# Performance work log

Measured on AMD Instinct MI355X. Metric: run time of the kernel, lower is better.

Reference implementation:

```python
import jax, jax.numpy as jnp
import numpy as np


def _conv(x, w, b, stride=1, pad=0):
    y = jax.lax.conv_general_dilated(
        x, w, (stride, stride), [(pad, pad), (pad, pad)],
        dimension_numbers=('NCHW', 'OIHW', 'NCHW'))
    return y + b[None, :, None, None]


def _channel_mask(x, w, b):
    # SE-style hard channel mask: GAP -> linear -> hard threshold at 0
    pooled = jnp.mean(x, axis=(2, 3))                 # [B, Cin]
    logits = pooled @ w.T + b                         # [B, Cout]
    return (logits > 0).astype(x.dtype)[:, :, None, None]


def _maxpool3(m):
    # 3x3 stride-1 dilation of the binary spatial mask
    return jax.lax.reduce_window(m, -jnp.inf, jax.lax.max,
                                 (1, 1, 3, 3), (1, 1, 1, 1),
                                 [(0, 0), (0, 0), (1, 1), (1, 1)])


def _hswish(x):
    return x * jax.nn.relu6(x + 3.0) / 6.0


def _coord_att(x, w1, b1, wh, bh, ww, bw):
    B, C, H, W = x.shape
    xh = jnp.mean(x, axis=3, keepdims=True)                         # [B,C,H,1]
    xw = jnp.mean(x, axis=2, keepdims=True).transpose(0, 1, 3, 2)   # [B,C,W,1]
    y = _hswish(_conv(jnp.concatenate([xh, xw], axis=2), w1, b1))   # [B,mip,H+W,1]
    yh, yw = y[:, :, :H], y[:, :, H:]
    ah = jax.nn.sigmoid(_conv(yh, wh, bh))                          # [B,C,H,1]
    aw = jax.nn.sigmoid(_conv(yw, ww, bw)).transpose(0, 1, 3, 2)    # [B,C,1,W]
    return x * ah * aw


def setup_inputs() -> dict:
    key = jax.random.key(0)
    ks = jax.random.split(key, 16)
    B, INP, WID, OUP, H, W, MIP = 16, 512, 128, 512, 56, 56, 16
    f32 = jnp.float32
    rn = lambda k, s, sc: jax.random.normal(k, s, f32) * sc
    return {
        'x': rn(ks[0], (B, INP, H, W), 1.0),
        # spatial mask unit (1x1 conv to 1-channel logits)
        'sm_w': rn(ks[1], (1, INP, 1, 1), 0.05), 'sm_b': jnp.zeros((1,), f32),
        # channel mask units (GAP + linear)
        'cm1_w': rn(ks[2], (WID, INP), 0.05), 'cm1_b': jnp.zeros((WID,), f32),
        'cm2_w': rn(ks[3], (WID, WID), 0.09), 'cm2_b': jnp.zeros((WID,), f32),
        'cm3_w': rn(ks[4], (OUP, WID), 0.09), 'cm3_b': jnp.zeros((OUP,), f32),
        # bottleneck convs
        'w1': rn(ks[5], (WID, INP, 1, 1), 0.044), 'b1': jnp.zeros((WID,), f32),
        'w2': rn(ks[6], (WID, WID, 3, 3), 0.029), 'b2': jnp.zeros((WID,), f32),
        'w3': rn(ks[7], (OUP, WID, 1, 1), 0.088), 'b3': jnp.zeros((OUP,), f32),
        # coordinate attention
        'ca_w1': rn(ks[8], (MIP, OUP, 1, 1), 0.044), 'ca_b1': jnp.zeros((MIP,), f32),
        'ca_wh': rn(ks[9], (OUP, MIP, 1, 1), 0.25), 'ca_bh': jnp.zeros((OUP,), f32),
        'ca_ww': rn(ks[10], (OUP, MIP, 1, 1), 0.25), 'ca_bw': jnp.zeros((OUP,), f32),
    }


def reference(x, sm_w, sm_b, cm1_w, cm1_b, cm2_w, cm2_b, cm3_w, cm3_b,
              w1, b1, w2, b2, w3, b3,
              ca_w1, ca_b1, ca_wh, ca_bh, ca_ww, ca_bw):
    identity = x
    # spatial masks: std + 3x3-dilated
    s_mask = (_conv(x, sm_w, sm_b) > 0).astype(x.dtype)   # [B,1,H,W]
    s_mask_dil = _maxpool3(s_mask)
    # conv1: 1x1 + ReLU, gated by channel mask 1 and dilated spatial mask
    cm1 = _channel_mask(x, cm1_w, cm1_b)
    h = jax.nn.relu(_conv(x, w1, b1)) * cm1 * s_mask_dil
    # conv2: 3x3 + ReLU, gated by channel mask 2 and std spatial mask
    cm2 = _channel_mask(h, cm2_w, cm2_b)
    h = jax.nn.relu(_conv(h, w2, b2, pad=1)) * cm2 * s_mask
    # conv3: 1x1, no activation, gated by channel mask 3 and std spatial mask
    cm3 = _channel_mask(h, cm3_w, cm3_b)
    h = _conv(h, w3, b3) * cm3 * s_mask
    # coordinate attention + residual
    out = _coord_att(h, ca_w1, ca_b1, ca_wh, ca_bh, ca_ww, ca_bw)
    return jax.nn.relu(out + identity)
```

## Files before the change

kernel.cpp:

```cpp
#include <hip/hip_runtime.h>

#define HWn 3136
#define W56 56
#define Bn  16
#define CIN0 512

typedef unsigned short ushortT;
typedef __attribute__((ext_vector_type(8))) short bf16x8;
typedef __attribute__((ext_vector_type(4))) float f32x4;

__device__ inline ushortT bf_hi(float v) {
    unsigned u = __float_as_uint(v);
    unsigned r = u + 0x7FFFu + ((u >> 16) & 1u);
    return (ushortT)(r >> 16);
}
__device__ inline float bf_f(ushortT h) { return __uint_as_float(((unsigned)h) << 16); }

__global__ __launch_bounds__(256) void pool_mean_kernel(const float* __restrict__ in,
                                                        float* __restrict__ out)
{
    int bc = blockIdx.x;
    const float* p = in + (size_t)bc * HWn;
    float s = 0.f;
    for (int i = threadIdx.x; i < HWn; i += 256) s += p[i];
#pragma unroll
    for (int off = 32; off > 0; off >>= 1) s += __shfl_down(s, off);
    __shared__ float red[4];
    if ((threadIdx.x & 63) == 0) red[threadIdx.x >> 6] = s;
    __syncthreads();
    if (threadIdx.x == 0) out[bc] = (red[0] + red[1] + red[2] + red[3]) / 3136.f;
}

__global__ void zero_kernel(float* __restrict__ p, int n)
{
    int i = blockIdx.x * 256 + threadIdx.x;
    if (i < n) p[i] = 0.f;
}

__global__ __launch_bounds__(256) void pool_meanT_kernel(const ushortT* __restrict__ hi,
        const ushortT* __restrict__ lo, float* __restrict__ pooled)
{
    int b = blockIdx.x, slice = blockIdx.y;
    int t = threadIdx.x;
    int c4 = (t & 31) * 4, rg = t >> 5;
    float a0 = 0.f, a1 = 0.f, a2 = 0.f, a3 = 0.f;
    for (int it = 0; it < 49; ++it) {
        int p = slice * 392 + rg + it * 8;
        size_t base = ((size_t)b * HWn + p) * 128 + c4;
        ushort4 h4 = *(const ushort4*)&hi[base];
        ushort4 l4 = *(const ushort4*)&lo[base];
        a0 += bf_f(h4.x) + bf_f(l4.x);
        a1 += bf_f(h4.y) + bf_f(l4.y);
        a2 += bf_f(h4.z) + bf_f(l4.z);
        a3 += bf_f(h4.w) + bf_f(l4.w);
    }
    __shared__ float red[8][128];
    red[rg][c4] = a0; red[rg][c4 + 1] = a1; red[rg][c4 + 2] = a2; red[rg][c4 + 3] = a3;
    __syncthreads();
    if (t < 128) {
        float s = 0.f;
#pragma unroll
        for (int g = 0; g < 8; ++g) s += red[g][t];
        atomicAdd(&pooled[b * 128 + t], s * (1.f / 3136.f));
    }
}

__global__ void chan_mask_kernel(const float* __restrict__ pooled, const float* __restrict__ Wm,
                                 const float* __restrict__ bias, float* __restrict__ mask,
                                 int Cin, int Cout)
{
    int b = blockIdx.x, o = threadIdx.x;
    if (o >= Cout) return;
    const float* pr = pooled + (size_t)b * Cin;
    const float* wr = Wm + (size_t)o * Cin;
    float s = bias[o];
    for (int c = 0; c < Cin; ++c) s = fmaf(pr[c], wr[c], s);
    mask[b * Cout + o] = (s > 0.f) ? 1.f : 0.f;
}

__global__ __launch_bounds__(256) void spatial_mask_kernel(const float* __restrict__ x,
        const float* __restrict__ smw, const float* __restrict__ smb, float* __restrict__ smask)
{
    __shared__ float ws[512];
    int b = blockIdx.x;
    for (int i = threadIdx.x; i < 512; i += 256) ws[i] = smw[i];
    __syncthreads();
    int p = blockIdx.y * 256 + threadIdx.x;
    if (p >= HWn) return;
    const float* xp = x + (size_t)b * CIN0 * HWn + p;
    float s = smb[0];
#pragma unroll 8
    for (int c = 0; c < CIN0; ++c) s = fmaf(xp[(size_t)c * HWn], ws[c], s);
    smask[b * HWn + p] = (s > 0.f) ? 1.f : 0.f;
}

__global__ __launch_bounds__(256) void dilate_kernel(const float* __restrict__ sm, float* __restrict__ sd)
{
    int b = blockIdx.x;
    int p = blockIdx.y * 256 + threadIdx.x;
    if (p >= HWn) return;
    int py = p / W56, px = p % W56;
    float m = 0.f;
    for (int dy = -1; dy <= 1; ++dy) {
        int sy = py + dy; if (sy < 0 || sy >= W56) continue;
        for (int dx = -1; dx <= 1; ++dx) {
            int sx = px + dx; if (sx < 0 || sx >= W56) continue;
            m = fmaxf(m, sm[b * HWn + sy * W56 + sx]);
        }
    }
    sd[b * HWn + p] = m;
}

__global__ void split_w_kernel(const float* __restrict__ w, ushortT* __restrict__ hi,
                               ushortT* __restrict__ lo, int n)
{
    int i = blockIdx.x * 256 + threadIdx.x;
    if (i >= n) return;
    float v = w[i];
    ushortT h = bf_hi(v);
    hi[i] = h;
    lo[i] = bf_hi(v - bf_f(h));
}

__global__ void split_w2_kernel(const float* __restrict__ w2, ushortT* __restrict__ hi,
                                ushortT* __restrict__ lo)
{
    int e = blockIdx.x * 256 + threadIdx.x;
    if (e >= 9 * 128 * 128) return;
    int c = e & 127, o = (e >> 7) & 127, tap = e >> 14;
    float v = w2[((size_t)o * 128 + c) * 9 + tap];
    ushortT h = bf_hi(v);
    hi[e] = h;
    lo[e] = bf_hi(v - bf_f(h));
}

template<int KC, int TAPS, bool RELU, bool IN_F32, bool OUT_F32>
__global__ __launch_bounds__(256) void mfma_conv_kernel(
    const float* __restrict__ in_f32,
    const ushortT* __restrict__ in_hi, const ushortT* __restrict__ in_lo,
    const ushortT* __restrict__ wh, const ushortT* __restrict__ wl,
    const float* __restrict__ bias, const float* __restrict__ cmask,
    const float* __restrict__ pmask,
    float* __restrict__ out_f32, ushortT* __restrict__ out_hi, ushortT* __restrict__ out_lo,
    int Cout)
{
    __shared__ __align__(16) ushortT As_hi[128 * 40], As_lo[128 * 40];
    __shared__ __align__(16) ushortT Bs_hi[128 * 40], Bs_lo[128 * 40];
    __shared__ float s_bias[128], s_cm[128];

    const int b  = blockIdx.z;
    const int o0 = blockIdx.y * 128;
    const int p0 = blockIdx.x * 128;
    const int tid = threadIdx.x;
    const int lane = tid & 63;
    const int g  = lane >> 4;
    const int lc = lane & 15;
    const int wid = tid >> 6;
    const int wm = wid >> 1, wn = wid & 1;

    if (tid < 128) {
        s_bias[tid] = bias[o0 + tid];
        s_cm[tid]   = cmask[b * Cout + o0 + tid];
    }

    int aoff[4], boff[4];
#pragma unroll
    for (int m = 0; m < 4; ++m) aoff[m] = (wm * 64 + m * 16 + lc) * 40 + g * 8;
#pragma unroll
    for (int n = 0; n < 4; ++n) {
        int pl = wn * 64 + n * 16 + lc;
        boff[n] = pl * 40 + ((g ^ (pl & 3)) * 8);
    }

    f32x4 acc[4][4];
#pragma unroll
    for (int m = 0; m < 4; ++m)
#pragma unroll
        for (int n = 0; n < 4; ++n) acc[m][n] = (f32x4){0.f, 0.f, 0.f, 0.f};

    for (int tap = 0; tap < TAPS; ++tap) {
        const int dy = (TAPS == 9) ? (tap / 3 - 1) : 0;
        const int dx = (TAPS == 9) ? (tap % 3 - 1) : 0;
        for (int kc = 0; kc < KC; kc += 32) {
            __syncthreads();
#pragma unroll
            for (int i = 0; i < 2; ++i) {
                int unit = tid + i * 256;
                int row = unit >> 2, ch = unit & 3;
                size_t srow = (TAPS == 9) ? ((size_t)tap * 128 + row) * 128
                                          : (size_t)(o0 + row) * KC;
                uint4 vh = *(const uint4*)(wh + srow + kc + ch * 8);
                uint4 vl = *(const uint4*)(wl + srow + kc + ch * 8);
                *(uint4*)&As_hi[row * 40 + ch * 8] = vh;
                *(uint4*)&As_lo[row * 40 + ch * 8] = vl;
            }
            if (IN_F32) {
                const float* inB = in_f32 + (size_t)b * KC * HWn;
#pragma unroll
                for (int j = 0; j < 4; ++j) {
                    int cr = (tid >> 5) + j * 8;
                    int p4 = (tid & 31) * 4;
                    float4 xv = make_float4(0.f, 0.f, 0.f, 0.f);
                    if (p0 + p4 < HWn)
                        xv = *(const float4*)&inB[(size_t)(kc + cr) * HWn + p0 + p4];
                    float vv[4] = {xv.x, xv.y, xv.z, xv.w};
#pragma unroll
                    for (int e = 0; e < 4; ++e) {
                        int prow = p4 + e;
                        ushortT h = bf_hi(vv[e]);
                        ushortT l = bf_hi(vv[e] - bf_f(h));
                        int kk = ((cr >> 3) ^ (prow & 3)) * 8 + (cr & 7);
                        Bs_hi[prow * 40 + kk] = h;
                        Bs_lo[prow * 40 + kk] = l;
                    }
                }
            } else {
#pragma unroll
                for (int i = 0; i < 2; ++i) {
                    int unit = tid + i * 256;
                    int row = unit >> 2, ch = unit & 3;
                    int pg = p0 + row;
                    int q = pg, valid;
                    if (TAPS == 9) {
                        int py = pg / 56, px = pg % 56;
                        int sy = py + dy, sx = px + dx;
                        valid = (pg < HWn) && (sy >= 0) && (sy < 56) && (sx >= 0) && (sx < 56);
                        q = sy * 56 + sx;
                    } else {
                        valid = (pg < HWn);
                    }
                    uint4 vh = make_uint4(0u, 0u, 0u, 0u), vl = vh;
                    if (valid) {
                        size_t sbase = ((size_t)b * HWn + q) * 128 + kc + ch * 8;
                        vh = *(const uint4*)(in_hi + sbase);
                        vl = *(const uint4*)(in_lo + sbase);
                    }
                    int chs = ch ^ (row & 3);
                    *(uint4*)&Bs_hi[row * 40 + chs * 8] = vh;
                    *(uint4*)&Bs_lo[row * 40 + chs * 8] = vl;
                }
            }
            __syncthreads();
            bf16x8 a_h[4], a_l[4];
#pragma unroll
            for (int m = 0; m < 4; ++m) {
                a_h[m] = *(const bf16x8*)&As_hi[aoff[m]];
                a_l[m] = *(const bf16x8*)&As_lo[aoff[m]];
            }
#pragma unroll
            for (int n = 0; n < 4; ++n) {
                bf16x8 b_h = *(const bf16x8*)&Bs_hi[boff[n]];
                bf16x8 b_l = *(const bf16x8*)&Bs_lo[boff[n]];
#pragma unroll
                for (int m = 0; m < 4; ++m) {
                    acc[m][n] = __builtin_amdgcn_mfma_f32_16x16x32_bf16(a_h[m], b_h, acc[m][n], 0, 0, 0);
                    acc[m][n] = __builtin_amdgcn_mfma_f32_16x16x32_bf16(a_h[m], b_l, acc[m][n], 0, 0, 0);
                    acc[m][n] = __builtin_amdgcn_mfma_f32_16x16x32_bf16(a_l[m], b_h, acc[m][n], 0, 0, 0);
                }
            }
        }
    }

#pragma unroll
    for (int m = 0; m < 4; ++m) {
        int ob = wm * 64 + m * 16 + g * 4;
        f32x4 b4 = *(const f32x4*)&s_bias[ob];
        f32x4 c4 = *(const f32x4*)&s_cm[ob];
#pragma unroll
        for (int n = 0; n < 4; ++n) {
            int p = p0 + wn * 64 + n * 16 + lc;
            if (p >= HWn) continue;
            float pm = pmask[b * HWn + p];
            float v[4];
#pragma unroll
            for (int r = 0; r < 4; ++r) {
                float t = acc[m][n][r] + b4[r];
                if (RELU) t = fmaxf(t, 0.f);
                v[r] = t * c4[r] * pm;
            }
            if (OUT_F32) {
#pragma unroll
                for (int r = 0; r < 4; ++r)
                    out_f32[((size_t)b * Cout + o0 + ob + r) * HWn + p] = v[r];
            } else {
                ushort4 H, L;
                H.x = bf_hi(v[0]); L.x = bf_hi(v[0] - bf_f(H.x));
                H.y = bf_hi(v[1]); L.y = bf_hi(v[1] - bf_f(H.y));
                H.z = bf_hi(v[2]); L.z = bf_hi(v[2] - bf_f(H.z));
                H.w = bf_hi(v[3]); L.w = bf_hi(v[3] - bf_f(H.w));
                size_t base = ((size_t)b * HWn + p) * 128 + ob;
                *(ushort4*)&out_hi[base] = H;
                *(ushort4*)&out_lo[base] = L;
            }
        }
    }
}

__global__ __launch_bounds__(128) void rowcol_mean_kernel(const float* __restrict__ h3,
        float* __restrict__ xh, float* __restrict__ xw)
{
    __shared__ float t[HWn];
    int bc = blockIdx.x;
    const float* p = h3 + (size_t)bc * HWn;
    for (int i = threadIdx.x; i < HWn; i += 128) t[i] = p[i];
    __syncthreads();
    int tid = threadIdx.x;
    if (tid < 56) {
        float s = 0.f;
#pragma unroll
        for (int i = 0; i < 56; ++i) s += t[tid * 56 + i];
        xh[(size_t)bc * 56 + tid] = s / 56.f;
    } else if (tid >= 64 && tid < 120) {
        int c = tid - 64;
        float s = 0.f;
#pragma unroll
        for (int i = 0; i < 56; ++i) s += t[i * 56 + c];
        xw[(size_t)bc * 56 + c] = s / 56.f;
    }
}

__global__ __launch_bounds__(256) void ca_y_kernel(const float* __restrict__ xh,
        const float* __restrict__ xw, const float* __restrict__ w1c,
        const float* __restrict__ b1c, float* __restrict__ y)
{
    int b = blockIdx.x;
    int t = blockIdx.y;
    __shared__ float src[512];
    __shared__ float part[16][17];
    for (int c = threadIdx.x; c < 512; c += 256)
        src[c] = (t < 56) ? xh[((size_t)b * 512 + c) * 56 + t]
                          : xw[((size_t)b * 512 + c) * 56 + (t - 56)];
    __syncthreads();
    int m  = threadIdx.x & 15;
    int cp = threadIdx.x >> 4;
    float s = 0.f;
#pragma unroll 8
    for (int i = 0; i < 32; ++i) {
        int c = cp * 32 + i;
        s = fmaf(w1c[(size_t)m * 512 + c], src[c], s);
    }
    part[m][cp] = s;
    __syncthreads();
    if (threadIdx.x < 16) {
        float v = b1c[threadIdx.x];
#pragma unroll
        for (int i = 0; i < 16; ++i) v += part[threadIdx.x][i];
        float r6 = fminf(fmaxf(v + 3.f, 0.f), 6.f);
        y[((size_t)b * 16 + threadIdx.x) * 112 + t] = v * r6 / 6.f;
    }
}

__global__ __launch_bounds__(512) void ca_a_kernel(const float* __restrict__ y,
        const float* __restrict__ wh, const float* __restrict__ bh,
        const float* __restrict__ wwp, const float* __restrict__ bw,
        float* __restrict__ ah, float* __restrict__ aw)
{
    int r = blockIdx.x;
    int side = blockIdx.y;
    int b = blockIdx.z;
    int o = threadIdx.x;
    __shared__ float ys[16];
    if (threadIdx.x < 16)
        ys[threadIdx.x] = y[((size_t)b * 16 + threadIdx.x) * 112 + side * 56 + r];
    __syncthreads();
    const float* wmat = side ? wwp : wh;
    float s = (side ? bw : bh)[o];
#pragma unroll
    for (int m = 0; m < 16; ++m) s = fmaf(wmat[o * 16 + m], ys[m], s);
    float sig = 1.f / (1.f + expf(-s));
    (side ? aw : ah)[((size_t)b * 512 + o) * 56 + r] = sig;
}

__global__ __launch_bounds__(256) void finalize_kernel(const float* __restrict__ x,
        const float* __restrict__ ah, const float* __restrict__ aw, float* __restrict__ out)
{
    int e = blockIdx.x * 256 + threadIdx.x;
    int pq = e % 784;
    int bc = e / 784;
    int p = pq * 4;
    int py = p / 56, px = p % 56;
    float4 h = *((const float4*)out + e);
    float4 xv = *((const float4*)x + e);
    float a_h = ah[(size_t)bc * 56 + py];
    float4 a_w = *(const float4*)&aw[(size_t)bc * 56 + px];
    float4 v;
    v.x = fmaxf(h.x * a_h * a_w.x + xv.x, 0.f);
    v.y = fmaxf(h.y * a_h * a_w.y + xv.y, 0.f);
    v.z = fmaxf(h.z * a_h * a_w.z + xv.z, 0.f);
    v.w = fmaxf(h.w * a_h * a_w.w + xv.w, 0.f);
    *((float4*)out + e) = v;
}

extern "C" void kernel_launch(void* const* d_in, const int* in_sizes, int n_in,
                              void* d_out, int out_size, void* d_ws, size_t ws_size,
                              hipStream_t stream)
{
    (void)in_sizes; (void)n_in; (void)out_size; (void)ws_size;
    const float* x     = (const float*)d_in[0];
    const float* sm_w  = (const float*)d_in[1];
    const float* sm_b  = (const float*)d_in[2];
    const float* cm1_w = (const float*)d_in[3];
    const float* cm1_b = (const float*)d_in[4];
    const float* cm2_w = (const float*)d_in[5];
    const float* cm2_b = (const float*)d_in[6];
    const float* cm3_w = (const float*)d_in[7];
    const float* cm3_b = (const float*)d_in[8];
    const float* w1    = (const float*)d_in[9];
    const float* b1    = (const float*)d_in[10];
    const float* w2    = (const float*)d_in[11];
    const float* b2    = (const float*)d_in[12];
    const float* w3    = (const float*)d_in[13];
    const float* b3    = (const float*)d_in[14];
    const float* ca_w1 = (const float*)d_in[15];
    const float* ca_b1 = (const float*)d_in[16];
    const float* ca_wh = (const float*)d_in[17];
    const float* ca_bh = (const float*)d_in[18];
    const float* ca_ww = (const float*)d_in[19];
    const float* ca_bw = (const float*)d_in[20];
    float* out = (float*)d_out;

    float* fp = (float*)d_ws;
    float* pooled_x  = fp;              fp += 8192;
    float* cm1m      = fp;              fp += 2048;
    float* smask     = fp;              fp += 50176;
    float* sdil      = fp;              fp += 50176;
    float* pooled_h1 = fp;              fp += 2048;
    float* cm2m      = fp;              fp += 2048;
    float* pooled_h2 = fp;              fp += 2048;
    float* cm3m      = fp;              fp += 8192;
    ushortT* up = (ushortT*)fp;
    ushortT* w1h = up;                  up += 65536;
    ushortT* w1l = up;                  up += 65536;
    ushortT* w2h = up;                  up += 147456;
    ushortT* w2l = up;                  up += 147456;
    ushortT* w3h = up;                  up += 65536;
    ushortT* w3l = up;                  up += 65536;
    ushortT* h1h = up;                  up += 6422528;
    ushortT* h1l = up;                  up += 6422528;
    ushortT* h2h = up;                  up += 6422528;
    ushortT* h2l = up;                  up += 6422528;
    float* xh  = (float*)h1h;
    float* xwm = xh + 458752;
    float* yb  = xwm + 458752;
    float* ah  = yb + 28672;
    float* aw  = ah + 458752;

    zero_kernel<<<8, 256, 0, stream>>>(pooled_h1, 2048);
    zero_kernel<<<8, 256, 0, stream>>>(pooled_h2, 2048);
    pool_mean_kernel<<<Bn * CIN0, 256, 0, stream>>>(x, pooled_x);
    chan_mask_kernel<<<Bn, 128, 0, stream>>>(pooled_x, cm1_w, cm1_b, cm1m, 512, 128);
    spatial_mask_kernel<<<dim3(Bn, 13), 256, 0, stream>>>(x, sm_w, sm_b, smask);
    dilate_kernel<<<dim3(Bn, 13), 256, 0, stream>>>(smask, sdil);
    split_w_kernel<<<256, 256, 0, stream>>>(w1, w1h, w1l, 65536);
    split_w2_kernel<<<576, 256, 0, stream>>>(w2, w2h, w2l);
    split_w_kernel<<<256, 256, 0, stream>>>(w3, w3h, w3l, 65536);

    mfma_conv_kernel<512, 1, true, true, false><<<dim3(25, 1, Bn), 256, 0, stream>>>(
        x, nullptr, nullptr, w1h, w1l, b1, cm1m, sdil, nullptr, h1h, h1l, 128);

    pool_meanT_kernel<<<dim3(Bn, 8), 256, 0, stream>>>(h1h, h1l, pooled_h1);
    chan_mask_kernel<<<Bn, 128, 0, stream>>>(pooled_h1, cm2_w, cm2_b, cm2m, 128, 128);

    mfma_conv_kernel<128, 9, true, false, false><<<dim3(25, 1, Bn), 256, 0, stream>>>(
        nullptr, h1h, h1l, w2h, w2l, b2, cm2m, smask, nullptr, h2h, h2l, 128);

    pool_meanT_kernel<<<dim3(Bn, 8), 256, 0, stream>>>(h2h, h2l, pooled_h2);
    chan_mask_kernel<<<Bn, 512, 0, stream>>>(pooled_h2, cm3_w, cm3_b, cm3m, 128, 512);

    mfma_conv_kernel<128, 1, false, false, true><<<dim3(25, 4, Bn), 256, 0, stream>>>(
        nullptr, h2h, h2l, w3h, w3l, b3, cm3m, smask, out, nullptr, nullptr, 512);

    rowcol_mean_kernel<<<Bn * 512, 128, 0, stream>>>(out, xh, xwm);
    ca_y_kernel<<<dim3(Bn, 112), 256, 0, stream>>>(xh, xwm, ca_w1, ca_b1, yb);
    ca_a_kernel<<<dim3(W56, 2, Bn), 512, 0, stream>>>(yb, ca_wh, ca_bh, ca_ww, ca_bw, ah, aw);
    finalize_kernel<<<25088, 256, 0, stream>>>(x, ah, aw, out);
}
```

Measured before the change: 663.5 us.

## Fuse spatial-mask logits with channel pooling and shrink conv tiles to 64 outputs

Replaces the separate global-average-pool and spatial-mask kernels with one tiled kernel that reads x once, computes partial spatial logits per 64-channel slice and per-channel sums via atomics, followed by a small threshold kernel. The MFMA conv kernel moves from 256-thread 128x128 tiles to 128-thread 64x128 tiles, doubling the grid. It also removes the LDS XOR swizzle and rewrites the fp32 input staging so each thread packs channel pairs. This should cut redundant passes over x and raise block count, but dropping the swizzle may bring back LDS bank conflicts and the partial-logit buffer adds extra traffic.

```diff
diff --git a/kernel.cpp b/kernel.cpp
--- a/kernel.cpp
+++ b/kernel.cpp
@@ -16,25 +16,83 @@
 }
 __device__ inline float bf_f(ushortT h) { return __uint_as_float(((unsigned)h) << 16); }
 
-__global__ __launch_bounds__(256) void pool_mean_kernel(const float* __restrict__ in,
-                                                        float* __restrict__ out)
-{
-    int bc = blockIdx.x;
-    const float* p = in + (size_t)bc * HWn;
-    float s = 0.f;
-    for (int i = threadIdx.x; i < HWn; i += 256) s += p[i];
-#pragma unroll
-    for (int off = 32; off > 0; off >>= 1) s += __shfl_down(s, off);
-    __shared__ float red[4];
-    if ((threadIdx.x & 63) == 0) red[threadIdx.x >> 6] = s;
-    __syncthreads();
-    if (threadIdx.x == 0) out[bc] = (red[0] + red[1] + red[2] + red[3]) / 3136.f;
-}
-
 __global__ void zero_kernel(float* __restrict__ p, int n)
 {
     int i = blockIdx.x * 256 + threadIdx.x;
     if (i < n) p[i] = 0.f;
+}
+
+__global__ __launch_bounds__(256) void mask_pool_kernel(
+    const float* __restrict__ x, const float* __restrict__ smw,
+    float* __restrict__ slog_part, float* __restrict__ pooled)
+{
+    __shared__ float s_t[64][129];
+    __shared__ float s_w[64];
+    __shared__ float s_slog[128];
+    __shared__ float s_pool[4][64];
+    const int b = blockIdx.z, ct = blockIdx.y, pt = blockIdx.x;
+    const int c0 = ct * 64, p0 = pt * 128;
+    const int t = threadIdx.x;
+    if (t < 64) s_w[t] = smw[c0 + t];
+    __syncthreads();
+    const int pi = t & 127, par = t >> 7;
+    const int p = p0 + pi;
+    const bool pv = (p < HWn);
+    const float* xb = x + ((size_t)b * 512 + c0) * HWn;
+    float sacc = 0.f;
+#pragma unroll 4
+    for (int rep = 0; rep < 32; ++rep) {
+        int ci = rep * 2 + par;
+        float v = pv ? xb[(size_t)ci * HWn + p] : 0.f;
+        s_t[ci][pi] = v;
+        sacc = fmaf(v, s_w[ci], sacc);
+    }
+    if (par == 0) s_slog[pi] = sacc;
+    __syncthreads();
+    if (par == 1) s_slog[pi] += sacc;
+    __syncthreads();
+    if (t < 128 && p0 + t < HWn)
+        slog_part[((size_t)b * 8 + ct) * HWn + p0 + t] = s_slog[t];
+    const int c = t & 63, pg = t >> 6;
+    float a = 0.f;
+#pragma unroll 8
+    for (int it = 0; it < 32; ++it) a += s_t[c][pg * 32 + it];
+    s_pool[pg], __syncthreads();
+    s_pool[pg][c] = a;
+    __syncthreads();
+    if (t < 64) {
+        float s = s_pool[0][t] + s_pool[1][t] + s_pool[2][t] + s_pool[3][t];
+        atomicAdd(&pooled[b * 512 + c0 + t], s * (1.f / 3136.f));
+    }
+}
+
+__global__ void thresh_kernel(const float* __restrict__ slog_part,
+                              const float* __restrict__ smb, float* __restrict__ smask)
+{
+    int e = blockIdx.x * 256 + threadIdx.x;
+    if (e >= Bn * HWn) return;
+    int b = e / HWn, p = e % HWn;
+    float s = smb[0];
+#pragma unroll
+    for (int i = 0; i < 8; ++i) s += slog_part[((size_t)b * 8 + i) * HWn + p];
+    smask[e] = (s > 0.f) ? 1.f : 0.f;
+}
+
+__global__ __launch_bounds__(256) void dilate_kernel(const float* __restrict__ sm, float* __restrict__ sd)
+{
+    int b = blockIdx.x;
+    int p = blockIdx.y * 256 + threadIdx.x;
+    if (p >= HWn) return;
+    int py = p / W56, px = p % W56;
+    float m = 0.f;
+    for (int dy = -1; dy <= 1; ++dy) {
+        int sy = py + dy; if (sy < 0 || sy >= W56) continue;
+        for (int dx = -1; dx <= 1; ++dx) {
+            int sx = px + dx; if (sx < 0 || sx >= W56) continue;
+            m = fmaxf(m, sm[b * HWn + sy * W56 + sx]);
+        }
+    }
+    sd[b * HWn + p] = m;
 }
 
 __global__ __launch_bounds__(256) void pool_meanT_kernel(const ushortT* __restrict__ hi,
@@ -78,39 +136,6 @@
     mask[b * Cout + o] = (s > 0.f) ? 1.f : 0.f;
 }
 
-__global__ __launch_bounds__(256) void spatial_mask_kernel(const float* __restrict__ x,
-        const float* __restrict__ smw, const float* __restrict__ smb, float* __restrict__ smask)
-{
-    __shared__ float ws[512];
-    int b = blockIdx.x;
-    for (int i = threadIdx.x; i < 512; i += 256) ws[i] = smw[i];
-    __syncthreads();
-    int p = blockIdx.y * 256 + threadIdx.x;
-    if (p >= HWn) return;
-    const float* xp = x + (size_t)b * CIN0 * HWn + p;
-    float s = smb[0];
-#pragma unroll 8
-    for (int c = 0; c < CIN0; ++c) s = fmaf(xp[(size_t)c * HWn], ws[c], s);
-    smask[b * HWn + p] = (s > 0.f) ? 1.f : 0.f;
-}
-
-__global__ __launch_bounds__(256) void dilate_kernel(const float* __restrict__ sm, float* __restrict__ sd)
-{
-    int b = blockIdx.x;
-    int p = blockIdx.y * 256 + threadIdx.x;
-    if (p >= HWn) return;
-    int py = p / W56, px = p % W56;
-    float m = 0.f;
-    for (int dy = -1; dy <= 1; ++dy) {
-        int sy = py + dy; if (sy < 0 || sy >= W56) continue;
-        for (int dx = -1; dx <= 1; ++dx) {
-            int sx = px + dx; if (sx < 0 || sx >= W56) continue;
-            m = fmaxf(m, sm[b * HWn + sy * W56 + sx]);
-        }
-    }
-    sd[b * HWn + p] = m;
-}
-
 __global__ void split_w_kernel(const float* __restrict__ w, ushortT* __restrict__ hi,
                                ushortT* __restrict__ lo, int n)
 {
@@ -135,7 +160,7 @@
 }
 
 template<int KC, int TAPS, bool RELU, bool IN_F32, bool OUT_F32>
-__global__ __launch_bounds__(256) void mfma_conv_kernel(
+__global__ __launch_bounds__(128) void mfma_conv_kernel(
     const float* __restrict__ in_f32,
     const ushortT* __restrict__ in_hi, const ushortT* __restrict__ in_lo,
     const ushortT* __restrict__ wh, const ushortT* __restrict__ wl,
@@ -144,33 +169,29 @@
     float* __restrict__ out_f32, ushortT* __restrict__ out_hi, ushortT* __restrict__ out_lo,
     int Cout)
 {
-    __shared__ __align__(16) ushortT As_hi[128 * 40], As_lo[128 * 40];
+    __shared__ __align__(16) ushortT As_hi[64 * 40], As_lo[64 * 40];
     __shared__ __align__(16) ushortT Bs_hi[128 * 40], Bs_lo[128 * 40];
-    __shared__ float s_bias[128], s_cm[128];
+    __shared__ float s_bias[64], s_cm[64];
 
     const int b  = blockIdx.z;
-    const int o0 = blockIdx.y * 128;
+    const int o0 = blockIdx.y * 64;
     const int p0 = blockIdx.x * 128;
     const int tid = threadIdx.x;
     const int lane = tid & 63;
     const int g  = lane >> 4;
     const int lc = lane & 15;
-    const int wid = tid >> 6;
-    const int wm = wid >> 1, wn = wid & 1;
-
-    if (tid < 128) {
+    const int wn = tid >> 6;
+
+    if (tid < 64) {
         s_bias[tid] = bias[o0 + tid];
         s_cm[tid]   = cmask[b * Cout + o0 + tid];
     }
 
     int aoff[4], boff[4];
 #pragma unroll
-    for (int m = 0; m < 4; ++m) aoff[m] = (wm * 64 + m * 16 + lc) * 40 + g * 8;
-#pragma unroll
-    for (int n = 0; n < 4; ++n) {
-        int pl = wn * 64 + n * 16 + lc;
-        boff[n] = pl * 40 + ((g ^ (pl & 3)) * 8);
-    }
+    for (int m = 0; m < 4; ++m) aoff[m] = (m * 16 + lc) * 40 + g * 8;
+#pragma unroll
+    for (int n = 0; n < 4; ++n) boff[n] = (wn * 64 + n * 16 + lc) * 40 + g * 8;
 
     f32x4 acc[4][4];
 #pragma unroll
@@ -185,42 +206,37 @@
             __syncthreads();
 #pragma unroll
             for (int i = 0; i < 2; ++i) {
-                int unit = tid + i * 256;
-                int row = unit >> 2, ch = unit & 3;
-                size_t srow = (TAPS == 9) ? ((size_t)tap * 128 + row) * 128
-                                          : (size_t)(o0 + row) * KC;
-                uint4 vh = *(const uint4*)(wh + srow + kc + ch * 8);
-                uint4 vl = *(const uint4*)(wl + srow + kc + ch * 8);
-                *(uint4*)&As_hi[row * 40 + ch * 8] = vh;
-                *(uint4*)&As_lo[row * 40 + ch * 8] = vl;
+                int u = tid + i * 128;
+                int row = u >> 2, ch = u & 3;
+                size_t srow = (TAPS == 9) ? (((size_t)tap * 128 + o0 + row) * 128 + kc)
+                                          : ((size_t)(o0 + row) * KC + kc);
+                *(uint4*)&As_hi[row * 40 + ch * 8] = *(const uint4*)(wh + srow + ch * 8);
+                *(uint4*)&As_lo[row * 40 + ch * 8] = *(const uint4*)(wl + srow + ch * 8);
             }
             if (IN_F32) {
                 const float* inB = in_f32 + (size_t)b * KC * HWn;
-#pragma unroll
-                for (int j = 0; j < 4; ++j) {
-                    int cr = (tid >> 5) + j * 8;
-                    int p4 = (tid & 31) * 4;
-                    float4 xv = make_float4(0.f, 0.f, 0.f, 0.f);
-                    if (p0 + p4 < HWn)
-                        xv = *(const float4*)&inB[(size_t)(kc + cr) * HWn + p0 + p4];
-                    float vv[4] = {xv.x, xv.y, xv.z, xv.w};
-#pragma unroll
-                    for (int e = 0; e < 4; ++e) {
-                        int prow = p4 + e;
-                        ushortT h = bf_hi(vv[e]);
-                        ushortT l = bf_hi(vv[e] - bf_f(h));
-                        int kk = ((cr >> 3) ^ (prow & 3)) * 8 + (cr & 7);
-                        Bs_hi[prow * 40 + kk] = h;
-                        Bs_lo[prow * 40 + kk] = l;
-                    }
+                const int p = tid;
+                const int gp = p0 + p;
+                const bool pv = (gp < HWn);
+                uint* bh32 = (uint*)Bs_hi;
+                uint* bl32 = (uint*)Bs_lo;
+#pragma unroll
+                for (int j = 0; j < 16; ++j) {
+                    float v0 = pv ? inB[(size_t)(kc + 2 * j) * HWn + gp] : 0.f;
+                    float v1 = pv ? inB[(size_t)(kc + 2 * j + 1) * HWn + gp] : 0.f;
+                    ushortT h0 = bf_hi(v0), h1 = bf_hi(v1);
+                    ushortT l0 = bf_hi(v0 - bf_f(h0)), l1 = bf_hi(v1 - bf_f(h1));
+                    bh32[p * 20 + j] = (uint)h0 | ((uint)h1 << 16);
+                    bl32[p * 20 + j] = (uint)l0 | ((uint)l1 << 16);
                 }
             } else {
 #pragma unroll
-                for (int i = 0; i < 2; ++i) {
-                    int unit = tid + i * 256;
-                    int row = unit >> 2, ch = unit & 3;
+                for (int i = 0; i < 4; ++i) {
+                    int u = tid + i * 128;
+                    int row = u >> 2, ch = u & 3;
                     int pg = p0 + row;
-                    int q = pg, valid;
+                    int q = pg;
+                    bool valid;
                     if (TAPS == 9) {
                         int py = pg / 56, px = pg % 56;
                         int sy = py + dy, sx = px + dx;
@@ -231,13 +247,12 @@
                     }
                     uint4 vh = make_uint4(0u, 0u, 0u, 0u), vl = vh;
                     if (valid) {
-                        size_t sbase = ((size_t)b * HWn + q) * 128 + kc + ch * 8;
-                        vh = *(const uint4*)(in_hi + sbase);
-                        vl = *(const uint4*)(in_lo + sbase);
+                        size_t sb = ((size_t)b * HWn + q) * KC + kc + ch * 8;
+                        vh = *(const uint4*)(in_hi + sb);
+                        vl = *(const uint4*)(in_lo + sb);
                     }
-                    int chs = ch ^ (row & 3);
-                    *(uint4*)&Bs_hi[row * 40 + chs * 8] = vh;
-                    *(uint4*)&Bs_lo[row * 40 + chs * 8] = vl;
+                    *(uint4*)&Bs_hi[row * 40 + ch * 8] = vh;
+                    *(uint4*)&Bs_lo[row * 40 + ch * 8] = vl;
                 }
             }
             __syncthreads();
@@ -263,7 +278,7 @@
 
 #pragma unroll
     for (int m = 0; m < 4; ++m) {
-        int ob = wm * 64 + m * 16 + g * 4;
+        int ob = m * 16 + g * 4;
         f32x4 b4 = *(const f32x4*)&s_bias[ob];
         f32x4 c4 = *(const f32x4*)&s_cm[ob];
 #pragma unroll
@@ -288,7 +303,7 @@
                 H.y = bf_hi(v[1]); L.y = bf_hi(v[1] - bf_f(H.y));
                 H.z = bf_hi(v[2]); L.z = bf_hi(v[2] - bf_f(H.z));
                 H.w = bf_hi(v[3]); L.w = bf_hi(v[3] - bf_f(H.w));
-                size_t base = ((size_t)b * HWn + p) * 128 + ob;
+                size_t base = ((size_t)b * HWn + p) * 128 + o0 + ob;
                 *(ushort4*)&out_hi[base] = H;
                 *(ushort4*)&out_lo[base] = L;
             }
@@ -421,13 +436,14 @@
 
     float* fp = (float*)d_ws;
     float* pooled_x  = fp;              fp += 8192;
+    float* pooled_h1 = fp;              fp += 2048;
+    float* pooled_h2 = fp;              fp += 2048;
     float* cm1m      = fp;              fp += 2048;
+    float* cm2m      = fp;              fp += 2048;
+    float* cm3m      = fp;              fp += 8192;
     float* smask     = fp;              fp += 50176;
     float* sdil      = fp;              fp += 50176;
-    float* pooled_h1 = fp;              fp += 2048;
-    float* cm2m      = fp;              fp += 2048;
-    float* pooled_h2 = fp;              fp += 2048;
-    float* cm3m      = fp;              fp += 8192;
+    float* slog_part = fp;              fp += 401408;
     ushortT* up = (ushortT*)fp;
     ushortT* w1h = up;                  up += 65536;
     ushortT* w1l = up;                  up += 65536;
@@ -445,29 +461,28 @@
     float* ah  = yb + 28672;
     float* aw  = ah + 458752;
 
-    zero_kernel<<<8, 256, 0, stream>>>(pooled_h1, 2048);
-    zero_kernel<<<8, 256, 0, stream>>>(pooled_h2, 2048);
-    pool_mean_kernel<<<Bn * CIN0, 256, 0, stream>>>(x, pooled_x);
+    zero_kernel<<<48, 256, 0, stream>>>(pooled_x, 12288);
+    mask_pool_kernel<<<dim3(25, 8, Bn), 256, 0, stream>>>(x, sm_w, slog_part, pooled_x);
+    thresh_kernel<<<196, 256, 0, stream>>>(slog_part, sm_b, smask);
+    dilate_kernel<<<dim3(Bn, 13), 256, 0, stream>>>(smask, sdil);
     chan_mask_kernel<<<Bn, 128, 0, stream>>>(pooled_x, cm1_w, cm1_b, cm1m, 512, 128);
-    spatial_mask_kernel<<<dim3(Bn, 13), 256, 0, stream>>>(x, sm_w, sm_b, smask);
-    dilate_kernel<<<dim3(Bn, 13), 256, 0, stream>>>(smask, sdil);
     split_w_kernel<<<256, 256, 0, stream>>>(w1, w1h, w1l, 65536);
     split_w2_kernel<<<576, 256, 0, stream>>>(w2, w2h, w2l);
     split_w_kernel<<<256, 256, 0, stream>>>(w3, w3h, w3l, 65536);
 
-    mfma_conv_kernel<512, 1, true, true, false><<<dim3(25, 1, Bn), 256, 0, stream>>>(
+    mfma_conv_kernel<512, 1, true, true, false><<<dim3(25, 2, Bn), 128, 0, stream>>>(
         x, nullptr, nullptr, w1h, w1l, b1, cm1m, sdil, nullptr, h1h, h1l, 128);
 
     pool_meanT_kernel<<<dim3(Bn, 8), 256, 0, stream>>>(h1h, h1l, pooled_h1);
     chan_mask_kernel<<<Bn, 128, 0, stream>>>(pooled_h1, cm2_w, cm2_b, cm2m, 128, 128);
 
-    mfma_conv_kernel<128, 9, true, false, false><<<dim3(25, 1, Bn), 256, 0, stream>>>(
+    mfma_conv_kernel<128, 9, true, false, false><<<dim3(25, 2, Bn), 128, 0, stream>>>(
         nullptr, h1h, h1l, w2h, w2l, b2, cm2m, smask, nullptr, h2h, h2l, 128);
 
     pool_meanT_kernel<<<dim3(Bn, 8), 256, 0, stream>>>(h2h, h2l, pooled_h2);
     chan_mask_kernel<<<Bn, 512, 0, stream>>>(pooled_h2, cm3_w, cm3_b, cm3m, 128, 512);
 
-    mfma_conv_kernel<128, 1, false, false, true><<<dim3(25, 4, Bn), 256, 0, stream>>>(
+    mfma_conv_kernel<128, 1, false, false, true><<<dim3(25, 8, Bn), 128, 0, stream>>>(
         nullptr, h2h, h2l, w3h, w3l, b3, cm3m, smask, out, nullptr, nullptr, 512);
 
     rowcol_mean_kernel<<<Bn * 512, 128, 0, stream>>>(out, xh, xwm);
```

After: 762.5 us. 14.9% more time.
